# Optimization experiments

Measured on AMD Instinct MI355X. Metric: run time of the kernel, lower is better.

## Reference

```python
import jax, jax.numpy as jnp
import numpy as np

N = 20000        # total nodes in batched graph
E = 160000       # edges (avg in-degree 8)
D_IN = 512
D_OUT = 512
MAX_DEG = 10
BN_EPS = 1e-5


def setup_inputs() -> dict:
    key = jax.random.key(0)
    ks = jax.random.split(key, 8)
    feats = jax.random.normal(ks[0], (N, D_IN), dtype=jnp.float32)
    src = jax.random.randint(ks[1], (E,), 0, N)
    dst = jax.random.randint(ks[2], (E,), 0, N)
    # Wl[d], bl[d]: lins_l for degree d (d>=1); Wl[0] is never used since h==0 for deg-0 nodes.
    # Wr[0], bl[0] play the role of lin_zero_deg; Wr[d] (d>=1) are the bias-free lins_r.
    Wl = jax.random.normal(ks[3], (MAX_DEG + 1, D_IN, D_OUT), dtype=jnp.float32) * 0.02
    Wr = jax.random.normal(ks[4], (MAX_DEG + 1, D_IN, D_OUT), dtype=jnp.float32) * 0.02
    bl = jax.random.normal(ks[5], (MAX_DEG + 1, D_OUT), dtype=jnp.float32) * 0.02
    gamma = jnp.ones((D_OUT,), dtype=jnp.float32)
    beta = jnp.zeros((D_OUT,), dtype=jnp.float32)
    return {"feats": feats, "src": src, "dst": dst, "Wl": Wl, "Wr": Wr,
            "bl": bl, "gamma": gamma, "beta": beta}


def reference(feats, src, dst, Wl, Wr, bl, gamma, beta):
    # 1) neighbor sum: h[v] = sum_{(u->v) in E} feats[u]   (fn.copy_u + fn.sum)
    h = jax.ops.segment_sum(feats[src], dst, num_segments=N)  # [N, D_IN]
    # in-degrees, clamped to max_degree
    deg = jnp.clip(jax.ops.segment_sum(jnp.ones((E,), dtype=jnp.int32), dst,
                                       num_segments=N), 0, MAX_DEG)  # [N]
    # 2) degree-bucketed linears, vectorized over the 11 buckets then gathered per node.
    #    out[n] = h[n] @ Wl[deg[n]] + feats[n] @ Wr[deg[n]] + bl[deg[n]]
    #    deg==0 nodes have h==0, so this reduces to lin_zero_deg(feats) = feats@Wr[0]+bl[0].
    Hl = jnp.einsum('ni,dio->dno', h, Wl)      # [11, N, D_OUT]
    Hr = jnp.einsum('ni,dio->dno', feats, Wr)  # [11, N, D_OUT]
    out = (Hl + Hr + bl[:, None, :])[deg, jnp.arange(N)]  # [N, D_OUT]
    # 3) batchnorm (training mode: batch stats, biased variance)
    mean = out.mean(axis=0)
    var = out.var(axis=0)
    out = (out - mean) * jax.lax.rsqrt(var + BN_EPS) * gamma + beta
    # 4) max aggregation over graph with self loops (fn.copy_u + fn.max)
    self_ids = jnp.arange(N)
    src_s = jnp.concatenate([src, self_ids])
    dst_s = jnp.concatenate([dst, self_ids])
    out = jax.ops.segment_max(out[src_s], dst_s, num_segments=N)  # [N, D_OUT]
    return out
```

## Files before the change

### kernel.cpp

```cpp
#include <hip/hip_runtime.h>
#include <hip/hip_bf16.h>
#include <stdint.h>

#define N_NODES 20000
#define N_EDGES 160000
#define DIN 512
#define DOUT 512
#define NBUCKET 11
#define KDIM 1024
#define MAXTILES 168

typedef float f32x4 __attribute__((ext_vector_type(4)));
typedef __attribute__((ext_vector_type(8))) __bf16 bf16x8;

static __device__ __forceinline__ unsigned short f2bf(float f) {
    union { float f; unsigned u; } v; v.f = f;
    unsigned r = v.u + 0x7FFFu + ((v.u >> 16) & 1u);
    return (unsigned short)(r >> 16);
}
static __device__ __forceinline__ float bflo(unsigned p) {
    union { unsigned u; float f; } v; v.u = p << 16; return v.f;
}
static __device__ __forceinline__ float bfhi(unsigned p) {
    union { unsigned u; float f; } v; v.u = p & 0xFFFF0000u; return v.f;
}
static __device__ __forceinline__ unsigned packbf(float lo, float hi) {
    return (unsigned)f2bf(lo) | ((unsigned)f2bf(hi) << 16);
}

static __device__ __forceinline__ void gload_lds16(const unsigned short* g, unsigned short* l) {
    __builtin_amdgcn_global_load_lds(
        (const __attribute__((address_space(1))) unsigned int*)g,
        (__attribute__((address_space(3))) unsigned int*)l, 16, 0, 0);
}

__global__ void k_deg(const int* __restrict__ dst, int* __restrict__ deg) {
    int e = blockIdx.x * 256 + threadIdx.x;
    if (e < N_EDGES) atomicAdd(&deg[dst[e]], 1);
}

__global__ void k_scan(const int* __restrict__ deg, int* __restrict__ offsets) {
    __shared__ int part[1024];
    int t = threadIdx.x;
    const int CH = 20;
    int s0 = t * CH, s1 = min(s0 + CH, N_NODES);
    int s = 0;
    for (int i = s0; i < s1; ++i) s += deg[i];
    part[t] = s; __syncthreads();
    for (int off = 1; off < 1024; off <<= 1) {
        int v = part[t];
        int a = (t >= off) ? part[t - off] : 0;
        __syncthreads();
        part[t] = v + a;
        __syncthreads();
    }
    int base = (t == 0) ? 0 : part[t - 1];
    for (int i = s0; i < s1; ++i) { offsets[i] = base; base += deg[i]; }
    if (t == 1023) offsets[N_NODES] = part[1023];
}

__global__ __launch_bounds__(256)
void k_bucket(const int* __restrict__ deg, int* __restrict__ bucket_cnt,
              int* __restrict__ bucket_nodes) {
    __shared__ int lhist[NBUCKET];
    __shared__ int lbase[NBUCKET];
    int t = threadIdx.x;
    if (t < NBUCKET) lhist[t] = 0;
    __syncthreads();
    int v = blockIdx.x * 256 + t;
    int d = -1, slot = 0;
    if (v < N_NODES) {
        d = min(deg[v], NBUCKET - 1);
        slot = atomicAdd(&lhist[d], 1);
    }
    __syncthreads();
    if (t < NBUCKET && lhist[t] > 0) lbase[t] = atomicAdd(&bucket_cnt[t], lhist[t]);
    __syncthreads();
    if (v < N_NODES) bucket_nodes[d * N_NODES + lbase[d] + slot] = v;
}

__global__ void k_tiles(const int* __restrict__ bucket_cnt, int2* __restrict__ tiles,
                        int* __restrict__ tile_cnt) {
    if (threadIdx.x != 0 || blockIdx.x != 0) return;
    int tc = 0;
    for (int d = 0; d < NBUCKET; ++d) {
        int c = bucket_cnt[d];
        for (int m0 = 0; m0 < c; m0 += 128) tiles[tc++] = make_int2(d, m0);
    }
    *tile_cnt = tc;
}

__global__ void k_scatter(const int* __restrict__ src, const int* __restrict__ dst,
                          const int* __restrict__ offsets, int* __restrict__ cursor,
                          int* __restrict__ eidx) {
    int e = blockIdx.x * 256 + threadIdx.x;
    if (e >= N_EDGES) return;
    int v = dst[e];
    int slot = atomicAdd(&cursor[v], 1);
    eidx[offsets[v] + slot] = src[e];
}

__global__ __launch_bounds__(64)
void k_cast(const float* __restrict__ feats, unsigned short* __restrict__ X) {
    int n = blockIdx.x;
    int col = threadIdx.x * 8;
    f32x4 a = *(const f32x4*)(feats + (size_t)n * DIN + col);
    f32x4 b = *(const f32x4*)(feats + (size_t)n * DIN + col + 4);
    uint4 p;
    p.x = packbf(a[0], a[1]); p.y = packbf(a[2], a[3]);
    p.z = packbf(b[0], b[1]); p.w = packbf(b[2], b[3]);
    *(uint4*)(X + (size_t)n * KDIM + DIN + col) = p;
}

__global__ __launch_bounds__(64)
void k_build_x(const int* __restrict__ eidx, const int* __restrict__ offsets,
               unsigned short* __restrict__ X) {
    int n = blockIdx.x;
    int col = threadIdx.x * 8;
    int s = offsets[n], e = offsets[n + 1];
    float acc[8] = {0, 0, 0, 0, 0, 0, 0, 0};
    for (int i = s; i < e; ++i) {
        int u = eidx[i];
        uint4 p = *(const uint4*)(X + (size_t)u * KDIM + DIN + col);
        acc[0] += bflo(p.x); acc[1] += bfhi(p.x);
        acc[2] += bflo(p.y); acc[3] += bfhi(p.y);
        acc[4] += bflo(p.z); acc[5] += bfhi(p.z);
        acc[6] += bflo(p.w); acc[7] += bfhi(p.w);
    }
    uint4 o;
    o.x = packbf(acc[0], acc[1]); o.y = packbf(acc[2], acc[3]);
    o.z = packbf(acc[4], acc[5]); o.w = packbf(acc[6], acc[7]);
    *(uint4*)(X + (size_t)n * KDIM + col) = o;
}

__global__ __launch_bounds__(256)
void k_wt(const float* __restrict__ Wl, const float* __restrict__ Wr,
          unsigned short* __restrict__ Wt) {
    __shared__ float tile[32][33];
    int d = blockIdx.z, n0 = blockIdx.y * 32, k0 = blockIdx.x * 32;
    int t = threadIdx.x;
    int c = t & 31, r0 = t >> 5;
    const float* srcp = (k0 < DIN) ? (Wl + (size_t)d * DIN * DOUT)
                                   : (Wr + (size_t)d * DIN * DOUT - (size_t)DIN * DOUT);
    for (int rr = 0; rr < 4; ++rr) {
        int r = r0 + rr * 8;
        tile[r][c] = srcp[(size_t)(k0 + r) * DOUT + n0 + c];
    }
    __syncthreads();
    for (int rr = 0; rr < 4; ++rr) {
        int r = r0 + rr * 8;
        Wt[((size_t)d * DOUT + n0 + r) * KDIM + k0 + c] = f2bf(tile[c][r]);
    }
}

__global__ __launch_bounds__(256)
void k_gemm(const unsigned short* __restrict__ X, const unsigned short* __restrict__ Wt,
            const int2* __restrict__ tiles, const int* __restrict__ tile_cnt,
            const int* __restrict__ bucket_nodes, const int* __restrict__ bucket_cnt,
            const float* __restrict__ bl, unsigned short* __restrict__ out_pre,
            float* __restrict__ bn_sum, float* __restrict__ bn_sumsq) {
    if ((int)blockIdx.x >= *tile_cnt) return;
    int2 td = tiles[blockIdx.x];
    int d = td.x, m0 = td.y;
    int cnt = bucket_cnt[d];
    int n0 = blockIdx.y * 128;

    __shared__ __align__(16) unsigned short As[128 * 32];
    __shared__ __align__(16) unsigned short Bs[128 * 32];
    __shared__ int ridS[128];
    __shared__ float colsum[128], colsq[128];

    int t = threadIdx.x;
    if (t < 128) {
        int gm = m0 + t;
        ridS[t] = (gm < cnt) ? bucket_nodes[d * N_NODES + gm] : -1;
        colsum[t] = 0.f; colsq[t] = 0.f;
    }
    __syncthreads();

    int lane = t & 63, w = t >> 6;
    int rrow = lane >> 2;
    int seg = lane & 3;

    int rA0 = ridS[w * 32 + rrow];
    int rA1 = ridS[w * 32 + 16 + rrow];
    const unsigned short* gA0 = X + (size_t)max(rA0, 0) * KDIM + seg * 8;
    const unsigned short* gA1 = X + (size_t)max(rA1, 0) * KDIM + seg * 8;
    const unsigned short* gB0 = Wt + ((size_t)d * DOUT + n0 + w * 32 + rrow) * KDIM + seg * 8;
    const unsigned short* gB1 = gB0 + (size_t)16 * KDIM;
    unsigned short* lA0 = &As[(w * 32) * 32];
    unsigned short* lA1 = &As[(w * 32 + 16) * 32];
    unsigned short* lB0 = &Bs[(w * 32) * 32];
    unsigned short* lB1 = &Bs[(w * 32 + 16) * 32];

    int wm = (w & 1) * 64, wn = (w >> 1) * 64;
    int lm = lane & 15, q = lane >> 4;

    f32x4 acc[4][4];
#pragma unroll
    for (int i = 0; i < 4; ++i)
#pragma unroll
        for (int j = 0; j < 4; ++j) acc[i][j] = (f32x4){0, 0, 0, 0};

    for (int kt = 0; kt < KDIM / 32; ++kt) {
        gload_lds16(gA0 + kt * 32, lA0);
        gload_lds16(gA1 + kt * 32, lA1);
        gload_lds16(gB0 + kt * 32, lB0);
        gload_lds16(gB1 + kt * 32, lB1);
        __syncthreads();

        bf16x8 af[4], bf[4];
#pragma unroll
        for (int mt = 0; mt < 4; ++mt)
            af[mt] = *(bf16x8*)&As[(wm + mt * 16 + lm) * 32 + q * 8];
#pragma unroll
        for (int nt = 0; nt < 4; ++nt)
            bf[nt] = *(bf16x8*)&Bs[(wn + nt * 16 + lm) * 32 + q * 8];
#pragma unroll
        for (int mt = 0; mt < 4; ++mt)
#pragma unroll
            for (int nt = 0; nt < 4; ++nt)
                acc[mt][nt] = __builtin_amdgcn_mfma_f32_16x16x32_bf16(af[mt], bf[nt], acc[mt][nt], 0, 0, 0);
        __syncthreads();
    }

    const float* blr = bl + d * DOUT + n0;
    float vsum[4] = {0, 0, 0, 0}, vsq[4] = {0, 0, 0, 0};
#pragma unroll
    for (int mt = 0; mt < 4; ++mt) {
#pragma unroll
        for (int r = 0; r < 4; ++r) {
            int row = wm + mt * 16 + q * 4 + r;
            int grow = ridS[row];
            if (grow < 0) continue;
            unsigned short* orow = out_pre + (size_t)grow * DOUT + n0;
#pragma unroll
            for (int nt = 0; nt < 4; ++nt) {
                int col = wn + nt * 16 + lm;
                float v = acc[mt][nt][r] + blr[col];
                orow[col] = f2bf(v);
                vsum[nt] += v; vsq[nt] += v * v;
            }
        }
    }
#pragma unroll
    for (int nt = 0; nt < 4; ++nt) {
        vsum[nt] += __shfl_xor(vsum[nt], 16, 64);
        vsum[nt] += __shfl_xor(vsum[nt], 32, 64);
        vsq[nt]  += __shfl_xor(vsq[nt], 16, 64);
        vsq[nt]  += __shfl_xor(vsq[nt], 32, 64);
    }
    if (q == 0) {
#pragma unroll
        for (int nt = 0; nt < 4; ++nt) {
            atomicAdd(&colsum[wn + nt * 16 + lm], vsum[nt]);
            atomicAdd(&colsq[wn + nt * 16 + lm], vsq[nt]);
        }
    }
    __syncthreads();
    if (t < 128) {
        atomicAdd(&bn_sum[n0 + t], colsum[t]);
        atomicAdd(&bn_sumsq[n0 + t], colsq[t]);
    }
}

__global__ void k_bnfinal(const float* __restrict__ bn_sum, const float* __restrict__ bn_sumsq,
                          const float* __restrict__ gamma, const float* __restrict__ beta,
                          float* __restrict__ scale, float* __restrict__ shift) {
    int c = blockIdx.x * 256 + threadIdx.x;
    if (c >= DOUT) return;
    float mean = bn_sum[c] / (float)N_NODES;
    float var = bn_sumsq[c] / (float)N_NODES - mean * mean;
    float rs = rsqrtf(var + 1e-5f);
    float sc = gamma[c] * rs;
    scale[c] = sc;
    shift[c] = beta[c] - mean * sc;
}

__global__ __launch_bounds__(64)
void k_max(const unsigned short* __restrict__ out_pre, const int* __restrict__ eidx,
           const int* __restrict__ offsets, const float* __restrict__ scale,
           const float* __restrict__ shift, float* __restrict__ out) {
    int n = blockIdx.x;
    int col = threadIdx.x * 8;
    float mx[8];
    {
        uint4 p = *(const uint4*)(out_pre + (size_t)n * DOUT + col);
        mx[0] = bflo(p.x); mx[1] = bfhi(p.x);
        mx[2] = bflo(p.y); mx[3] = bfhi(p.y);
        mx[4] = bflo(p.z); mx[5] = bfhi(p.z);
        mx[6] = bflo(p.w); mx[7] = bfhi(p.w);
    }
    int s = offsets[n], e = offsets[n + 1];
    for (int i = s; i < e; ++i) {
        int u = eidx[i];
        uint4 p = *(const uint4*)(out_pre + (size_t)u * DOUT + col);
        mx[0] = fmaxf(mx[0], bflo(p.x)); mx[1] = fmaxf(mx[1], bfhi(p.x));
        mx[2] = fmaxf(mx[2], bflo(p.y)); mx[3] = fmaxf(mx[3], bfhi(p.y));
        mx[4] = fmaxf(mx[4], bflo(p.z)); mx[5] = fmaxf(mx[5], bfhi(p.z));
        mx[6] = fmaxf(mx[6], bflo(p.w)); mx[7] = fmaxf(mx[7], bfhi(p.w));
    }
    f32x4 sc0 = *(const f32x4*)(scale + col);
    f32x4 sc1 = *(const f32x4*)(scale + col + 4);
    f32x4 sh0 = *(const f32x4*)(shift + col);
    f32x4 sh1 = *(const f32x4*)(shift + col + 4);
    f32x4 r0, r1;
    r0[0] = mx[0] * sc0[0] + sh0[0]; r0[1] = mx[1] * sc0[1] + sh0[1];
    r0[2] = mx[2] * sc0[2] + sh0[2]; r0[3] = mx[3] * sc0[3] + sh0[3];
    r1[0] = mx[4] * sc1[0] + sh1[0]; r1[1] = mx[5] * sc1[1] + sh1[1];
    r1[2] = mx[6] * sc1[2] + sh1[2]; r1[3] = mx[7] * sc1[3] + sh1[3];
    *(f32x4*)(out + (size_t)n * DOUT + col) = r0;
    *(f32x4*)(out + (size_t)n * DOUT + col + 4) = r1;
}

extern "C" void kernel_launch(void* const* d_in, const int* in_sizes, int n_in,
                              void* d_out, int out_size, void* d_ws, size_t ws_size,
                              hipStream_t stream) {
    const float* feats = (const float*)d_in[0];
    const int*   src   = (const int*)d_in[1];
    const int*   dst   = (const int*)d_in[2];
    const float* Wl    = (const float*)d_in[3];
    const float* Wr    = (const float*)d_in[4];
    const float* bl    = (const float*)d_in[5];
    const float* gamma = (const float*)d_in[6];
    const float* beta  = (const float*)d_in[7];
    float* out = (float*)d_out;

    char* ws = (char*)d_ws;
    size_t off = 0;
    auto alloc = [&](size_t bytes) -> void* {
        off = (off + 255) & ~(size_t)255;
        void* p = ws + off;
        off += bytes;
        return p;
    };

    int*   deg        = (int*)alloc(N_NODES * 4);
    int*   cursor     = (int*)alloc(N_NODES * 4);
    int*   bucket_cnt = (int*)alloc(16 * 4);
    float* bn_sum     = (float*)alloc(DOUT * 4);
    float* bn_sumsq   = (float*)alloc(DOUT * 4);
    size_t zbytes = off;

    int* offsets      = (int*)alloc((N_NODES + 1) * 4);
    int* bucket_nodes = (int*)alloc((size_t)NBUCKET * N_NODES * 4);
    int* eidx         = (int*)alloc(N_EDGES * 4);
    int2* tiles       = (int2*)alloc(MAXTILES * 8);
    int* tile_cnt     = (int*)alloc(4);
    float* scale      = (float*)alloc(DOUT * 4);
    float* shift      = (float*)alloc(DOUT * 4);
    unsigned short* X  = (unsigned short*)alloc((size_t)N_NODES * KDIM * 2);
    unsigned short* Wt = (unsigned short*)alloc((size_t)NBUCKET * DOUT * KDIM * 2);
    unsigned short* out_pre = (unsigned short*)alloc((size_t)N_NODES * DOUT * 2);

    hipMemsetAsync(d_ws, 0, zbytes, stream);

    k_deg<<<(N_EDGES + 255) / 256, 256, 0, stream>>>(dst, deg);
    k_scan<<<1, 1024, 0, stream>>>(deg, offsets);
    k_bucket<<<(N_NODES + 255) / 256, 256, 0, stream>>>(deg, bucket_cnt, bucket_nodes);
    k_tiles<<<1, 64, 0, stream>>>(bucket_cnt, tiles, tile_cnt);
    k_scatter<<<(N_EDGES + 255) / 256, 256, 0, stream>>>(src, dst, offsets, cursor, eidx);
    k_cast<<<N_NODES, 64, 0, stream>>>(feats, X);
    k_build_x<<<N_NODES, 64, 0, stream>>>(eidx, offsets, X);
    k_wt<<<dim3(KDIM / 32, DOUT / 32, NBUCKET), 256, 0, stream>>>(Wl, Wr, Wt);
    k_gemm<<<dim3(MAXTILES, 4), 256, 0, stream>>>(
        X, Wt, tiles, tile_cnt, bucket_nodes, bucket_cnt, bl, out_pre, bn_sum, bn_sumsq);
    k_bnfinal<<<2, 256, 0, stream>>>(bn_sum, bn_sumsq, gamma, beta, scale, shift);
    k_max<<<N_NODES, 64, 0, stream>>>(out_pre, eidx, offsets, scale, shift, out);
}
```

Baseline: 268.9 us.

## Merge prep kernels, widen GEMM K-tile with XOR swizzle, fold BN finalize into max

The cast and weight-transpose kernels are merged into one launch, and the BN finalize kernel is removed: each k_max thread now computes scale and shift itself from the sums. The GEMM K-tile doubles from 32 to 64, halving barrier count, and adds an XOR swizzle on LDS slots to avoid bank conflicts. The gather loops in build_x and max are unrolled by two to keep more loads in flight. In exchange, LDS use rises and every k_max block redundantly recomputes the per-column rsqrt.

```diff
diff --git a/kernel.cpp b/kernel.cpp
--- a/kernel.cpp
+++ b/kernel.cpp
@@ -9,6 +9,9 @@
 #define NBUCKET 11
 #define KDIM 1024
 #define MAXTILES 168
+#define BN_EPS 1e-5f
+#define CAST_BLOCKS (N_NODES / 4)
+#define WT_BLOCKS ((KDIM / 32) * (DOUT / 32) * NBUCKET)
 
 typedef float f32x4 __attribute__((ext_vector_type(4)));
 typedef __attribute__((ext_vector_type(8))) __bf16 bf16x8;
@@ -100,16 +103,41 @@
     eidx[offsets[v] + slot] = src[e];
 }
 
-__global__ __launch_bounds__(64)
-void k_cast(const float* __restrict__ feats, unsigned short* __restrict__ X) {
-    int n = blockIdx.x;
-    int col = threadIdx.x * 8;
-    f32x4 a = *(const f32x4*)(feats + (size_t)n * DIN + col);
-    f32x4 b = *(const f32x4*)(feats + (size_t)n * DIN + col + 4);
-    uint4 p;
-    p.x = packbf(a[0], a[1]); p.y = packbf(a[2], a[3]);
-    p.z = packbf(b[0], b[1]); p.w = packbf(b[2], b[3]);
-    *(uint4*)(X + (size_t)n * KDIM + DIN + col) = p;
+__global__ __launch_bounds__(256)
+void k_prep(const float* __restrict__ feats, const float* __restrict__ Wl,
+            const float* __restrict__ Wr, unsigned short* __restrict__ X,
+            unsigned short* __restrict__ Wt) {
+    int b = blockIdx.x;
+    int t = threadIdx.x;
+    if (b < CAST_BLOCKS) {
+        int n = b * 4 + (t >> 6);
+        int col = (t & 63) * 8;
+        f32x4 a = *(const f32x4*)(feats + (size_t)n * DIN + col);
+        f32x4 c = *(const f32x4*)(feats + (size_t)n * DIN + col + 4);
+        uint4 p;
+        p.x = packbf(a[0], a[1]); p.y = packbf(a[2], a[3]);
+        p.z = packbf(c[0], c[1]); p.w = packbf(c[2], c[3]);
+        *(uint4*)(X + (size_t)n * KDIM + DIN + col) = p;
+        return;
+    }
+    __shared__ float tile[32][33];
+    int idx = b - CAST_BLOCKS;
+    int d = idx / (32 * 16);
+    int rem = idx % (32 * 16);
+    int k0 = (rem & 31) * 32;
+    int n0 = (rem >> 5) * 32;
+    int c = t & 31, r0 = t >> 5;
+    const float* srcp = (k0 < DIN) ? (Wl + (size_t)d * DIN * DOUT)
+                                   : (Wr + (size_t)d * DIN * DOUT - (size_t)DIN * DOUT);
+    for (int rr = 0; rr < 4; ++rr) {
+        int r = r0 + rr * 8;
+        tile[r][c] = srcp[(size_t)(k0 + r) * DOUT + n0 + c];
+    }
+    __syncthreads();
+    for (int rr = 0; rr < 4; ++rr) {
+        int r = r0 + rr * 8;
+        Wt[((size_t)d * DOUT + n0 + r) * KDIM + k0 + c] = f2bf(tile[c][r]);
+    }
 }
 
 __global__ __launch_bounds__(64)
@@ -118,39 +146,29 @@
     int n = blockIdx.x;
     int col = threadIdx.x * 8;
     int s = offsets[n], e = offsets[n + 1];
-    float acc[8] = {0, 0, 0, 0, 0, 0, 0, 0};
-    for (int i = s; i < e; ++i) {
+    float a0[8] = {0,0,0,0,0,0,0,0}, a1[8] = {0,0,0,0,0,0,0,0};
+    int i = s;
+    for (; i + 1 < e; i += 2) {
+        int u0 = eidx[i], u1 = eidx[i + 1];
+        uint4 p = *(const uint4*)(X + (size_t)u0 * KDIM + DIN + col);
+        uint4 q = *(const uint4*)(X + (size_t)u1 * KDIM + DIN + col);
+        a0[0] += bflo(p.x); a0[1] += bfhi(p.x); a0[2] += bflo(p.y); a0[3] += bfhi(p.y);
+        a0[4] += bflo(p.z); a0[5] += bfhi(p.z); a0[6] += bflo(p.w); a0[7] += bfhi(p.w);
+        a1[0] += bflo(q.x); a1[1] += bfhi(q.x); a1[2] += bflo(q.y); a1[3] += bfhi(q.y);
+        a1[4] += bflo(q.z); a1[5] += bfhi(q.z); a1[6] += bflo(q.w); a1[7] += bfhi(q.w);
+    }
+    if (i < e) {
         int u = eidx[i];
         uint4 p = *(const uint4*)(X + (size_t)u * KDIM + DIN + col);
-        acc[0] += bflo(p.x); acc[1] += bfhi(p.x);
-        acc[2] += bflo(p.y); acc[3] += bfhi(p.y);
-        acc[4] += bflo(p.z); acc[5] += bfhi(p.z);
-        acc[6] += bflo(p.w); acc[7] += bfhi(p.w);
+        a0[0] += bflo(p.x); a0[1] += bfhi(p.x); a0[2] += bflo(p.y); a0[3] += bfhi(p.y);
+        a0[4] += bflo(p.z); a0[5] += bfhi(p.z); a0[6] += bflo(p.w); a0[7] += bfhi(p.w);
     }
     uint4 o;
-    o.x = packbf(acc[0], acc[1]); o.y = packbf(acc[2], acc[3]);
-    o.z = packbf(acc[4], acc[5]); o.w = packbf(acc[6], acc[7]);
+    o.x = packbf(a0[0] + a1[0], a0[1] + a1[1]);
+    o.y = packbf(a0[2] + a1[2], a0[3] + a1[3]);
+    o.z = packbf(a0[4] + a1[4], a0[5] + a1[5]);
+    o.w = packbf(a0[6] + a1[6], a0[7] + a1[7]);
     *(uint4*)(X + (size_t)n * KDIM + col) = o;
-}
-
-__global__ __launch_bounds__(256)
-void k_wt(const float* __restrict__ Wl, const float* __restrict__ Wr,
-          unsigned short* __restrict__ Wt) {
-    __shared__ float tile[32][33];
-    int d = blockIdx.z, n0 = blockIdx.y * 32, k0 = blockIdx.x * 32;
-    int t = threadIdx.x;
-    int c = t & 31, r0 = t >> 5;
-    const float* srcp = (k0 < DIN) ? (Wl + (size_t)d * DIN * DOUT)
-                                   : (Wr + (size_t)d * DIN * DOUT - (size_t)DIN * DOUT);
-    for (int rr = 0; rr < 4; ++rr) {
-        int r = r0 + rr * 8;
-        tile[r][c] = srcp[(size_t)(k0 + r) * DOUT + n0 + c];
-    }
-    __syncthreads();
-    for (int rr = 0; rr < 4; ++rr) {
-        int r = r0 + rr * 8;
-        Wt[((size_t)d * DOUT + n0 + r) * KDIM + k0 + c] = f2bf(tile[c][r]);
-    }
 }
 
 __global__ __launch_bounds__(256)
@@ -165,8 +183,8 @@
     int cnt = bucket_cnt[d];
     int n0 = blockIdx.y * 128;
 
-    __shared__ __align__(16) unsigned short As[128 * 32];
-    __shared__ __align__(16) unsigned short Bs[128 * 32];
+    __shared__ __align__(16) unsigned short As[128 * 64];
+    __shared__ __align__(16) unsigned short Bs[128 * 64];
     __shared__ int ridS[128];
     __shared__ float colsum[128], colsq[128];
 
@@ -179,22 +197,27 @@
     __syncthreads();
 
     int lane = t & 63, w = t >> 6;
-    int rrow = lane >> 2;
-    int seg = lane & 3;
-
-    int rA0 = ridS[w * 32 + rrow];
-    int rA1 = ridS[w * 32 + 16 + rrow];
-    const unsigned short* gA0 = X + (size_t)max(rA0, 0) * KDIM + seg * 8;
-    const unsigned short* gA1 = X + (size_t)max(rA1, 0) * KDIM + seg * 8;
-    const unsigned short* gB0 = Wt + ((size_t)d * DOUT + n0 + w * 32 + rrow) * KDIM + seg * 8;
-    const unsigned short* gB1 = gB0 + (size_t)16 * KDIM;
-    unsigned short* lA0 = &As[(w * 32) * 32];
-    unsigned short* lA1 = &As[(w * 32 + 16) * 32];
-    unsigned short* lB0 = &Bs[(w * 32) * 32];
-    unsigned short* lB1 = &Bs[(w * 32 + 16) * 32];
+    int r = lane >> 3;
+    int s = lane & 7;
+    int sg = s ^ r;
+
+    const unsigned short* gA[4];
+    const unsigned short* gB[4];
+    unsigned short* lA[4];
+    unsigned short* lB[4];
+#pragma unroll
+    for (int j = 0; j < 4; ++j) {
+        int row = w * 32 + j * 8 + r;
+        int rid = max(ridS[row], 0);
+        gA[j] = X + (size_t)rid * KDIM + sg * 8;
+        gB[j] = Wt + ((size_t)d * DOUT + n0 + row) * KDIM + sg * 8;
+        lA[j] = &As[(w * 32 + j * 8) * 64];
+        lB[j] = &Bs[(w * 32 + j * 8) * 64];
+    }
 
     int wm = (w & 1) * 64, wn = (w >> 1) * 64;
     int lm = lane & 15, q = lane >> 4;
+    int sw = lm & 7;
 
     f32x4 acc[4][4];
 #pragma unroll
@@ -202,25 +225,30 @@
 #pragma unroll
         for (int j = 0; j < 4; ++j) acc[i][j] = (f32x4){0, 0, 0, 0};
 
-    for (int kt = 0; kt < KDIM / 32; ++kt) {
-        gload_lds16(gA0 + kt * 32, lA0);
-        gload_lds16(gA1 + kt * 32, lA1);
-        gload_lds16(gB0 + kt * 32, lB0);
-        gload_lds16(gB1 + kt * 32, lB1);
+    for (int kt = 0; kt < KDIM / 64; ++kt) {
+#pragma unroll
+        for (int j = 0; j < 4; ++j) {
+            gload_lds16(gA[j] + kt * 64, lA[j]);
+            gload_lds16(gB[j] + kt * 64, lB[j]);
+        }
         __syncthreads();
 
-        bf16x8 af[4], bf[4];
-#pragma unroll
-        for (int mt = 0; mt < 4; ++mt)
-            af[mt] = *(bf16x8*)&As[(wm + mt * 16 + lm) * 32 + q * 8];
-#pragma unroll
-        for (int nt = 0; nt < 4; ++nt)
-            bf[nt] = *(bf16x8*)&Bs[(wn + nt * 16 + lm) * 32 + q * 8];
-#pragma unroll
-        for (int mt = 0; mt < 4; ++mt)
+#pragma unroll
+        for (int kk = 0; kk < 2; ++kk) {
+            int slot = (kk * 4 + q) ^ sw;
+            bf16x8 af[4], bfr[4];
+#pragma unroll
+            for (int mt = 0; mt < 4; ++mt)
+                af[mt] = *(bf16x8*)&As[(wm + mt * 16 + lm) * 64 + slot * 8];
 #pragma unroll
             for (int nt = 0; nt < 4; ++nt)
-                acc[mt][nt] = __builtin_amdgcn_mfma_f32_16x16x32_bf16(af[mt], bf[nt], acc[mt][nt], 0, 0, 0);
+                bfr[nt] = *(bf16x8*)&Bs[(wn + nt * 16 + lm) * 64 + slot * 8];
+#pragma unroll
+            for (int mt = 0; mt < 4; ++mt)
+#pragma unroll
+                for (int nt = 0; nt < 4; ++nt)
+                    acc[mt][nt] = __builtin_amdgcn_mfma_f32_16x16x32_bf16(af[mt], bfr[nt], acc[mt][nt], 0, 0, 0);
+        }
         __syncthreads();
     }
 
@@ -229,15 +257,15 @@
 #pragma unroll
     for (int mt = 0; mt < 4; ++mt) {
 #pragma unroll
-        for (int r = 0; r < 4; ++r) {
-            int row = wm + mt * 16 + q * 4 + r;
+        for (int rr = 0; rr < 4; ++rr) {
+            int row = wm + mt * 16 + q * 4 + rr;
             int grow = ridS[row];
             if (grow < 0) continue;
             unsigned short* orow = out_pre + (size_t)grow * DOUT + n0;
 #pragma unroll
             for (int nt = 0; nt < 4; ++nt) {
                 int col = wn + nt * 16 + lm;
-                float v = acc[mt][nt][r] + blr[col];
+                float v = acc[mt][nt][rr] + blr[col];
                 orow[col] = f2bf(v);
                 vsum[nt] += v; vsq[nt] += v * v;
             }
@@ -264,35 +292,35 @@
     }
 }
 
-__global__ void k_bnfinal(const float* __restrict__ bn_sum, const float* __restrict__ bn_sumsq,
-                          const float* __restrict__ gamma, const float* __restrict__ beta,
-                          float* __restrict__ scale, float* __restrict__ shift) {
-    int c = blockIdx.x * 256 + threadIdx.x;
-    if (c >= DOUT) return;
-    float mean = bn_sum[c] / (float)N_NODES;
-    float var = bn_sumsq[c] / (float)N_NODES - mean * mean;
-    float rs = rsqrtf(var + 1e-5f);
-    float sc = gamma[c] * rs;
-    scale[c] = sc;
-    shift[c] = beta[c] - mean * sc;
-}
-
 __global__ __launch_bounds__(64)
 void k_max(const unsigned short* __restrict__ out_pre, const int* __restrict__ eidx,
-           const int* __restrict__ offsets, const float* __restrict__ scale,
-           const float* __restrict__ shift, float* __restrict__ out) {
+           const int* __restrict__ offsets, const float* __restrict__ bn_sum,
+           const float* __restrict__ bn_sumsq, const float* __restrict__ gamma,
+           const float* __restrict__ beta, float* __restrict__ out) {
     int n = blockIdx.x;
     int col = threadIdx.x * 8;
     float mx[8];
     {
         uint4 p = *(const uint4*)(out_pre + (size_t)n * DOUT + col);
-        mx[0] = bflo(p.x); mx[1] = bfhi(p.x);
-        mx[2] = bflo(p.y); mx[3] = bfhi(p.y);
-        mx[4] = bflo(p.z); mx[5] = bfhi(p.z);
-        mx[6] = bflo(p.w); mx[7] = bfhi(p.w);
+        mx[0] = bflo(p.x); mx[1] = bfhi(p.x); mx[2] = bflo(p.y); mx[3] = bfhi(p.y);
+        mx[4] = bflo(p.z); mx[5] = bfhi(p.z); mx[6] = bflo(p.w); mx[7] = bfhi(p.w);
     }
     int s = offsets[n], e = offsets[n + 1];
-    for (int i = s; i < e; ++i) {
+    int i = s;
+    for (; i + 1 < e; i += 2) {
+        int u0 = eidx[i], u1 = eidx[i + 1];
+        uint4 p = *(const uint4*)(out_pre + (size_t)u0 * DOUT + col);
+        uint4 qq = *(const uint4*)(out_pre + (size_t)u1 * DOUT + col);
+        mx[0] = fmaxf(mx[0], fmaxf(bflo(p.x), bflo(qq.x)));
+        mx[1] = fmaxf(mx[1], fmaxf(bfhi(p.x), bfhi(qq.x)));
+        mx[2] = fmaxf(mx[2], fmaxf(bflo(p.y), bflo(qq.y)));
+        mx[3] = fmaxf(mx[3], fmaxf(bfhi(p.y), bfhi(qq.y)));
+        mx[4] = fmaxf(mx[4], fmaxf(bflo(p.z), bflo(qq.z)));
+        mx[5] = fmaxf(mx[5], fmaxf(bfhi(p.z), bfhi(qq.z)));
+        mx[6] = fmaxf(mx[6], fmaxf(bflo(p.w), bflo(qq.w)));
+        mx[7] = fmaxf(mx[7], fmaxf(bfhi(p.w), bfhi(qq.w)));
+    }
+    if (i < e) {
         int u = eidx[i];
         uint4 p = *(const uint4*)(out_pre + (size_t)u * DOUT + col);
         mx[0] = fmaxf(mx[0], bflo(p.x)); mx[1] = fmaxf(mx[1], bfhi(p.x));
@@ -300,15 +328,18 @@
         mx[4] = fmaxf(mx[4], bflo(p.z)); mx[5] = fmaxf(mx[5], bfhi(p.z));
         mx[6] = fmaxf(mx[6], bflo(p.w)); mx[7] = fmaxf(mx[7], bfhi(p.w));
     }
-    f32x4 sc0 = *(const f32x4*)(scale + col);
-    f32x4 sc1 = *(const f32x4*)(scale + col + 4);
-    f32x4 sh0 = *(const f32x4*)(shift + col);
-    f32x4 sh1 = *(const f32x4*)(shift + col + 4);
+    const float inv_n = 1.0f / (float)N_NODES;
     f32x4 r0, r1;
-    r0[0] = mx[0] * sc0[0] + sh0[0]; r0[1] = mx[1] * sc0[1] + sh0[1];
-    r0[2] = mx[2] * sc0[2] + sh0[2]; r0[3] = mx[3] * sc0[3] + sh0[3];
-    r1[0] = mx[4] * sc1[0] + sh1[0]; r1[1] = mx[5] * sc1[1] + sh1[1];
-    r1[2] = mx[6] * sc1[2] + sh1[2]; r1[3] = mx[7] * sc1[3] + sh1[3];
+#pragma unroll
+    for (int jj = 0; jj < 8; ++jj) {
+        int c = col + jj;
+        float mean = bn_sum[c] * inv_n;
+        float var = bn_sumsq[c] * inv_n - mean * mean;
+        float sc = gamma[c] * rsqrtf(var + BN_EPS);
+        float sh = beta[c] - mean * sc;
+        float v = mx[jj] * sc + sh;
+        if (jj < 4) r0[jj] = v; else r1[jj - 4] = v;
+    }
     *(f32x4*)(out + (size_t)n * DOUT + col) = r0;
     *(f32x4*)(out + (size_t)n * DOUT + col + 4) = r1;
 }
@@ -347,8 +378,6 @@
     int* eidx         = (int*)alloc(N_EDGES * 4);
     int2* tiles       = (int2*)alloc(MAXTILES * 8);
     int* tile_cnt     = (int*)alloc(4);
-    float* scale      = (float*)alloc(DOUT * 4);
-    float* shift      = (float*)alloc(DOUT * 4);
     unsigned short* X  = (unsigned short*)alloc((size_t)N_NODES * KDIM * 2);
     unsigned short* Wt = (unsigned short*)alloc((size_t)NBUCKET * DOUT * KDIM * 2);
     unsigned short* out_pre = (unsigned short*)alloc((size_t)N_NODES * DOUT * 2);
@@ -360,11 +389,9 @@
     k_bucket<<<(N_NODES + 255) / 256, 256, 0, stream>>>(deg, bucket_cnt, bucket_nodes);
     k_tiles<<<1, 64, 0, stream>>>(bucket_cnt, tiles, tile_cnt);
     k_scatter<<<(N_EDGES + 255) / 256, 256, 0, stream>>>(src, dst, offsets, cursor, eidx);
-    k_cast<<<N_NODES, 64, 0, stream>>>(feats, X);
+    k_prep<<<CAST_BLOCKS + WT_BLOCKS, 256, 0, stream>>>(feats, Wl, Wr, X, Wt);
     k_build_x<<<N_NODES, 64, 0, stream>>>(eidx, offsets, X);
-    k_wt<<<dim3(KDIM / 32, DOUT / 32, NBUCKET), 256, 0, stream>>>(Wl, Wr, Wt);
     k_gemm<<<dim3(MAXTILES, 4), 256, 0, stream>>>(
         X, Wt, tiles, tile_cnt, bucket_nodes, bucket_cnt, bl, out_pre, bn_sum, bn_sumsq);
-    k_bnfinal<<<2, 256, 0, stream>>>(bn_sum, bn_sumsq, gamma, beta, scale, shift);
-    k_max<<<N_NODES, 64, 0, stream>>>(out_pre, eidx, offsets, scale, shift, out);
-}
+    k_max<<<N_NODES, 64, 0, stream>>>(out_pre, eidx, offsets, bn_sum, bn_sumsq, gamma, beta, out);
+}
```

Measured after the change: 261.7 us. -2.7%, faster.
